# Optimization experiments

Hardware: AMD Instinct MI355X
Metric: run time of the kernel (lower is better)

The kernel has to match this reference:

```python
import jax, jax.numpy as jnp
import numpy as np

N_HEAD = 16

def setup_inputs() -> dict:
    key = jax.random.key(0)
    ks = jax.random.split(key, 6)
    C = 1024
    B, T, Tp = 8, 1024, 64
    s = 0.02
    return {
        "x": jax.random.normal(ks[0], (B, T, C), jnp.float32),
        "prefix_embd": jax.random.normal(ks[1], (B, Tp, C), jnp.float32),
        "w_attn": jax.random.normal(ks[2], (C, 3 * C), jnp.float32) * s,
        "b_attn": jnp.zeros((3 * C,), jnp.float32),
        "w_prefix": jax.random.normal(ks[3], (C, 3 * C), jnp.float32) * s,
        "b_prefix": jnp.zeros((3 * C,), jnp.float32),
        "w_proj": jax.random.normal(ks[4], (C, C), jnp.float32) * s,
        "b_proj": jnp.zeros((C,), jnp.float32),
    }

def _heads(t, H):
    B, T, C = t.shape
    return t.reshape(B, T, H, C // H).transpose(0, 2, 1, 3)  # (B,H,T,d)

def reference(x, prefix_embd, w_attn, b_attn, w_prefix, b_prefix, w_proj, b_proj):
    B, T, C = x.shape
    H = N_HEAD
    d = C // H
    Tp = prefix_embd.shape[1]
    scale = 1.0 / jnp.sqrt(jnp.asarray(d, x.dtype))

    qkv = x @ w_attn + b_attn
    q, k, v = (_heads(t, H) for t in jnp.split(qkv, 3, axis=2))  # (B,H,T,d)

    pqkv = prefix_embd @ w_prefix + b_prefix
    _, k_p, v_p = (_heads(t, H) for t in jnp.split(pqkv, 3, axis=2))  # (B,H,Tp,d)

    causal = jnp.tril(jnp.ones((T, T), bool))  # bias buffer slice
    neg_inf = jnp.asarray(float("-inf"), x.dtype)

    att = jnp.einsum("bhqd,bhkd->bhqk", q, k) * scale
    att = jnp.where(causal[None, None], att, neg_inf)
    att = jax.nn.softmax(att, axis=-1)

    att_p = jnp.einsum("bhqd,bhkd->bhqk", q, k_p) * scale
    att_p = jnp.where(causal[:, :Tp][None, None], att_p, neg_inf)
    att_p = jax.nn.softmax(att_p, axis=-1)

    y = jnp.einsum("bhqk,bhkd->bhqd", att_p, v_p) + jnp.einsum("bhqk,bhkd->bhqd", att, v)
    y = y.transpose(0, 2, 1, 3).reshape(B, T, C)
    return y @ w_proj + b_proj
```

## Files before the change

kernel.cpp:

```cpp
#include <hip/hip_runtime.h>
#include <hip/hip_bf16.h>
#include <cstdint>
#include <cstddef>

typedef __bf16 bf16_t;
typedef bf16_t bf16x8 __attribute__((ext_vector_type(8)));
typedef bf16_t bf16x4 __attribute__((ext_vector_type(4)));
typedef float f32x4 __attribute__((ext_vector_type(4)));

#define NB 8
#define NT 1024
#define NC 1024
#define NH 16
#define ND 64
#define NTP 64

__global__ __launch_bounds__(256) void k_cast2(const float* __restrict__ a, bf16_t* __restrict__ da,
                                               int n4a,
                                               const float* __restrict__ b2, bf16_t* __restrict__ db,
                                               int n4b) {
    int i = blockIdx.x * 256 + threadIdx.x;
    if (i < n4a) {
        float4 f = ((const float4*)a)[i];
        bf16x4 o;
        o[0] = (bf16_t)f.x; o[1] = (bf16_t)f.y; o[2] = (bf16_t)f.z; o[3] = (bf16_t)f.w;
        ((bf16x4*)da)[i] = o;
    } else {
        int j = i - n4a;
        if (j < n4b) {
            float4 f = ((const float4*)b2)[j];
            bf16x4 o;
            o[0] = (bf16_t)f.x; o[1] = (bf16_t)f.y; o[2] = (bf16_t)f.z; o[3] = (bf16_t)f.w;
            ((bf16x4*)db)[j] = o;
        }
    }
}

__global__ __launch_bounds__(256) void k_transpose3(const float* __restrict__ s0, bf16_t* __restrict__ d0,
                                                    const float* __restrict__ s1, bf16_t* __restrict__ d1,
                                                    const float* __restrict__ s2, bf16_t* __restrict__ d2) {
    __shared__ float tile[32][33];
    const int z = blockIdx.z;
    const float* src = (z == 0) ? s0 : (z == 1) ? s1 : s2;
    bf16_t* dst = (z == 0) ? d0 : (z == 1) ? d1 : d2;
    const int N = (z == 2) ? NC : 3 * NC;
    const int K = NC;
    if (z == 2 && blockIdx.x >= 32) return;
    int nt = blockIdx.x, kt = blockIdx.y;
    int tx = threadIdx.x & 31;
    int ty = threadIdx.x >> 5;
#pragma unroll
    for (int i = 0; i < 4; i++) {
        int r = ty + i * 8;
        tile[r][tx] = src[(size_t)(kt * 32 + r) * N + nt * 32 + tx];
    }
    __syncthreads();
#pragma unroll
    for (int i = 0; i < 4; i++) {
        int r = ty + i * 8;
        dst[(size_t)(nt * 32 + r) * K + kt * 32 + tx] = (bf16_t)tile[tx][r];
    }
}

template <int OMODE, int TSH>
__global__ __launch_bounds__(256) void k_gemm_f(const bf16_t* __restrict__ A,
                                                const bf16_t* __restrict__ BT,
                                                const float* __restrict__ bias,
                                                void* __restrict__ Cout,
                                                int M, int N, int K) {
    __shared__ bf16_t As[128 * 72];
    __shared__ bf16_t Bs[128 * 72];
    const int tid = threadIdx.x;
    const int lane = tid & 63;
    const int wave = tid >> 6;
    const int quad = lane >> 4;
    const int l15 = lane & 15;
    const int wm = (wave >> 1) * 64;
    const int wn = (wave & 1) * 64;
    const size_t rowA0 = (size_t)blockIdx.y * 128;
    const size_t colB0 = (size_t)blockIdx.x * 128;

    const f32x4 fz = {0.f, 0.f, 0.f, 0.f};
    f32x4 acc[4][4];
#pragma unroll
    for (int i = 0; i < 4; i++)
#pragma unroll
        for (int j = 0; j < 4; j++) acc[i][j] = fz;

    for (int k0 = 0; k0 < K; k0 += 64) {
        __syncthreads();
#pragma unroll
        for (int i = 0; i < 4; i++) {
            int c = tid + i * 256;
            int r = c >> 3;
            int kc = (c & 7) * 8;
            uint4 av = *(const uint4*)(A + (rowA0 + r) * (size_t)K + k0 + kc);
            *(uint4*)(&As[r * 72 + kc]) = av;
            uint4 bv = *(const uint4*)(BT + (colB0 + r) * (size_t)K + k0 + kc);
            *(uint4*)(&Bs[r * 72 + kc]) = bv;
        }
        __syncthreads();
#pragma unroll
        for (int kk = 0; kk < 2; kk++) {
            bf16x8 af[4], bfr[4];
#pragma unroll
            for (int i = 0; i < 4; i++)
                af[i] = *(const bf16x8*)(&As[(wm + i * 16 + l15) * 72 + kk * 32 + quad * 8]);
#pragma unroll
            for (int j = 0; j < 4; j++)
                bfr[j] = *(const bf16x8*)(&Bs[(wn + j * 16 + l15) * 72 + kk * 32 + quad * 8]);
#pragma unroll
            for (int i = 0; i < 4; i++)
#pragma unroll
                for (int j = 0; j < 4; j++)
                    acc[i][j] = __builtin_amdgcn_mfma_f32_16x16x32_bf16(af[i], bfr[j], acc[i][j], 0, 0, 0);
        }
    }
    const bool vpath = (OMODE == 2) && (colB0 >= (size_t)(2 * NC));
#pragma unroll
    for (int i = 0; i < 4; i++) {
        size_t row = rowA0 + wm + i * 16 + quad * 4;
#pragma unroll
        for (int j = 0; j < 4; j++) {
            int col = (int)colB0 + wn + j * 16 + l15;
            float bv = bias[col];
            if (vpath) {
                int hh = (col - 2 * NC) >> 6;
                int dd = col & 63;
                int bb = (int)(row >> TSH);
                int tt = (int)row & ((1 << TSH) - 1);
                int tileBase = (bb * NH + hh) * (1 << (TSH - 6)) + (tt >> 6);
                size_t chunkrow = (size_t)tileBase * 4 + (dd >> 4);
                size_t addr = chunkrow * (size_t)N + 2 * NC + (dd & 15) * 64 + (tt & 63);
                bf16x4 vv;
#pragma unroll
                for (int r = 0; r < 4; r++) vv[r] = (bf16_t)(acc[i][j][r] + bv);
                *(bf16x4*)((bf16_t*)Cout + addr) = vv;
            } else {
#pragma unroll
                for (int r = 0; r < 4; r++) {
                    float v = acc[i][j][r] + bv;
                    if (OMODE == 1)
                        ((float*)Cout)[(row + r) * (size_t)N + col] = v;
                    else
                        ((bf16_t*)Cout)[(row + r) * (size_t)N + col] = (bf16_t)v;
                }
            }
        }
    }
}


#define LOADREGS(KB, VCB)                                                            \
    rk0 = *(const uint4*)((KB) + (size_t)(tid >> 3) * 3072 + (tid & 7) * 8);         \
    rv0 = *(const uint4*)((VCB) + (size_t)(tid >> 7) * 3072 + (tid & 127) * 8);

#define STAGE(KS, VS)                                                \
    *(uint4*)(&(KS)[(tid >> 3) * 72 + (tid & 7) * 8]) = rk0;         \
    *(uint4*)(&(VS)[(tid >> 3) * 72 + (tid & 7) * 8]) = rv0;

#define QK(KS, Sj, j)                                                                  \
    Sj = __builtin_amdgcn_mfma_f32_16x16x32_bf16(                                      \
        aq0, *(const bf16x8*)(&(KS)[((j) * 16 + l15) * 72 + quad * 8]), Sj, 0, 0, 0);  \
    Sj = __builtin_amdgcn_mfma_f32_16x16x32_bf16(                                      \
        aq1, *(const bf16x8*)(&(KS)[((j) * 16 + l15) * 72 + 32 + quad * 8]), Sj, 0, 0, 0);

#define EXPJ(Sj, j, BL, LACC)                                           \
    {                                                                   \
        const int n_ = (j) * 16 + l15;                                  \
        _Pragma("unroll") for (int r_ = 0; r_ < 4; r_++) {              \
            float p_ = __expf(Sj[r_] * scale);                          \
            if (n_ > (BL) + r_) p_ = 0.f;                               \
            Sj[r_] = p_;                                                \
            LACC[r_] += p_;                                             \
        }                                                               \
    }

#define PSTORE(Sj, j)                                                   \
    _Pragma("unroll") for (int r_ = 0; r_ < 4; r_++)                    \
        P[(quad * 4 + r_) * 72 + (j) * 16 + l15] = (bf16_t)Sj[r_];

#define PV(VS, Oj, j)                                                                  \
    Oj = __builtin_amdgcn_mfma_f32_16x16x32_bf16(                                      \
        ap0, *(const bf16x8*)(&(VS)[((j) * 16 + l15) * 72 + quad * 8]), Oj, 0, 0, 0);  \
    Oj = __builtin_amdgcn_mfma_f32_16x16x32_bf16(                                      \
        ap1, *(const bf16x8*)(&(VS)[((j) * 16 + l15) * 72 + 32 + quad * 8]), Oj, 0, 0, 0);

#define PROC(KS, VS, BL, LACC, O0, O1, O2, O3)                          \
    {                                                                   \
        f32x4 S0 = fz, S1 = fz, S2 = fz, S3 = fz;                       \
        __builtin_amdgcn_s_setprio(1);                                  \
        QK(KS, S0, 0) QK(KS, S1, 1) QK(KS, S2, 2) QK(KS, S3, 3)         \
        __builtin_amdgcn_s_setprio(0);                                  \
        EXPJ(S0, 0, BL, LACC) EXPJ(S1, 1, BL, LACC)                     \
        EXPJ(S2, 2, BL, LACC) EXPJ(S3, 3, BL, LACC)                     \
        PSTORE(S0, 0) PSTORE(S1, 1) PSTORE(S2, 2) PSTORE(S3, 3)         \
        __builtin_amdgcn_s_waitcnt(0xc07f);             \
        __builtin_amdgcn_wave_barrier();                                \
        bf16x8 ap0 = *(const bf16x8*)(&P[l15 * 72 + quad * 8]);         \
        bf16x8 ap1 = *(const bf16x8*)(&P[l15 * 72 + 32 + quad * 8]);    \
        __builtin_amdgcn_s_setprio(1);                                  \
        PV(VS, O0, 0) PV(VS, O1, 1) PV(VS, O2, 2) PV(VS, O3, 3)         \
        __builtin_amdgcn_s_setprio(0);                                  \
    }

#define STORE_O(Oj, Pj, j)                                                            \
    _Pragma("unroll") for (int r_ = 0; r_ < 4; r_++) {                                \
        float v_ = Oj[r_] * lmv[r_] + Pj[r_] * lpv[r_];                               \
        y[(qrow0 + quad * 4 + r_) * NC + h * 64 + (j) * 16 + l15] = (bf16_t)v_;       \
    }

__global__ __launch_bounds__(512, 2) void k_attn11(const bf16_t* __restrict__ qkv,
                                                   const bf16_t* __restrict__ pqkv,
                                                   bf16_t* __restrict__ y) {
    const int qt = (NT / 128 - 1) - blockIdx.x;
    const int h = blockIdx.y;
    const int b = blockIdx.z;
    const int TMAX = 2 * qt + 1;

    __shared__ bf16_t Ks0[64 * 72], Ks1[64 * 72];
    __shared__ bf16_t Vs0[64 * 72], Vs1[64 * 72];
    __shared__ bf16_t Ps[8][16 * 72];

    const int tid = threadIdx.x;
    const int lane = tid & 63;
    const int wave = tid >> 6;
    const int quad = lane >> 4;
    const int l15 = lane & 15;
    const float scale = 0.125f;

    const size_t qrow0 = (size_t)b * NT + (size_t)qt * 128 + wave * 16;
    const int qoff = qt * 128 + wave * 16 + quad * 4;
    bf16_t* P = Ps[wave];

    const bf16_t* Kmain = qkv + (size_t)(b * NT) * 3072 + NC + h * 64;
    const bf16_t* Vmain = qkv + (size_t)(b * NH + h) * 16 * 4 * 3072 + 2 * NC;
    const bf16_t* Vpre  = pqkv + (size_t)(b * NH + h) * 4 * 3072 + 2 * NC;

    bf16x8 aq0 = *(const bf16x8*)(qkv + (qrow0 + l15) * 3072 + h * 64 + quad * 8);
    bf16x8 aq1 = *(const bf16x8*)(qkv + (qrow0 + l15) * 3072 + h * 64 + 32 + quad * 8);

    const f32x4 fz = {0.f, 0.f, 0.f, 0.f};
    f32x4 Om0 = fz, Om1 = fz, Om2 = fz, Om3 = fz;
    f32x4 Op0 = fz, Op1 = fz, Op2 = fz, Op3 = fz;
    f32x4 Lm = fz, Lp = fz;
    uint4 rk0, rv0;

    LOADREGS(pqkv + (size_t)(b * NTP) * 3072 + NC + h * 64, Vpre)
    STAGE(Ks0, Vs0)
    LOADREGS(Kmain, Vmain)
    __syncthreads();
    PROC(Ks0, Vs0, qoff, Lp, Op0, Op1, Op2, Op3)
    STAGE(Ks1, Vs1)
    LOADREGS(Kmain + (size_t)64 * 3072, Vmain + 4 * 3072)

    for (int t = 0; t <= TMAX; t++) {
        __syncthreads();
        bf16_t* KSc = (t & 1) ? Ks0 : Ks1;
        bf16_t* VSc = (t & 1) ? Vs0 : Vs1;
        if (t < TMAX) {
            bf16_t* KSn = (t & 1) ? Ks1 : Ks0;
            bf16_t* VSn = (t & 1) ? Vs1 : Vs0;
            STAGE(KSn, VSn)
        }
        if (t + 1 < TMAX) {
            LOADREGS(Kmain + ((size_t)(t + 2) * 64) * 3072, Vmain + (size_t)(t + 2) * 4 * 3072)
        }
        PROC(KSc, VSc, qoff - t * 64, Lm, Om0, Om1, Om2, Om3)
    }

    f32x4 lmv, lpv;
#pragma unroll
    for (int r = 0; r < 4; r++) {
        float vm = Lm[r], vpr = Lp[r];
#pragma unroll
        for (int off = 1; off < 16; off <<= 1) {
            vm += __shfl_xor(vm, off, 64);
            vpr += __shfl_xor(vpr, off, 64);
        }
        lmv[r] = 1.0f / vm;
        lpv[r] = 1.0f / vpr;
    }

    STORE_O(Om0, Op0, 0) STORE_O(Om1, Op1, 1) STORE_O(Om2, Op2, 2) STORE_O(Om3, Op3, 3)
}

extern "C" void kernel_launch(void* const* d_in, const int* in_sizes, int n_in,
                              void* d_out, int out_size, void* d_ws, size_t ws_size,
                              hipStream_t stream) {
    (void)in_sizes; (void)n_in; (void)out_size; (void)ws_size;
    const float* x        = (const float*)d_in[0];
    const float* prefix   = (const float*)d_in[1];
    const float* w_attn   = (const float*)d_in[2];
    const float* b_attn   = (const float*)d_in[3];
    const float* w_prefix = (const float*)d_in[4];
    const float* b_prefix = (const float*)d_in[5];
    const float* w_proj   = (const float*)d_in[6];
    const float* b_proj   = (const float*)d_in[7];
    float* out = (float*)d_out;

    char* p = (char*)d_ws;
    auto carve = [&](size_t bytes) {
        char* q = p;
        p += (bytes + 255) & ~(size_t)255;
        return q;
    };
    bf16_t* xb   = (bf16_t*)carve((size_t)NB * NT * NC * 2);
    bf16_t* pb   = (bf16_t*)carve((size_t)NB * NTP * NC * 2);
    bf16_t* wTa  = (bf16_t*)carve((size_t)3 * NC * NC * 2);
    bf16_t* wTp  = (bf16_t*)carve((size_t)3 * NC * NC * 2);
    bf16_t* wTpr = (bf16_t*)carve((size_t)NC * NC * 2);
    bf16_t* qkv  = (bf16_t*)carve((size_t)NB * NT * 3 * NC * 2);
    bf16_t* pqkv = (bf16_t*)carve((size_t)NB * NTP * 3 * NC * 2);
    bf16_t* yb   = (bf16_t*)carve((size_t)NB * NT * NC * 2);

    const int n4a = NB * NT * NC / 4, n4b = NB * NTP * NC / 4;
    k_cast2<<<(n4a + n4b + 255) / 256, 256, 0, stream>>>(x, xb, n4a, prefix, pb, n4b);
    k_transpose3<<<dim3(3 * NC / 32, NC / 32, 3), 256, 0, stream>>>(w_attn, wTa, w_prefix, wTp,
                                                                    w_proj, wTpr);
    k_gemm_f<2, 10><<<dim3(3 * NC / 128, NB * NT / 128), 256, 0, stream>>>(
        xb, wTa, b_attn, qkv, NB * NT, 3 * NC, NC);
    k_gemm_f<2, 6><<<dim3(3 * NC / 128, NB * NTP / 128), 256, 0, stream>>>(
        pb, wTp, b_prefix, pqkv, NB * NTP, 3 * NC, NC);
    k_attn11<<<dim3(NT / 128, NH, NB), 512, 0, stream>>>(qkv, pqkv, yb);
    k_gemm_f<1, 6><<<dim3(NC / 128, NB * NT / 128), 256, 0, stream>>>(
        yb, wTpr, b_proj, out, NB * NT, NC, NC);
}
```

Before: 307.9 us.

## Merge QKV and prefix GEMMs into one launch and remap workgroups across XCDs

Combines the main QKV projection and the prefix projection into a single GEMM launch of 24x68 workgroups, which removes one kernel launch and the tail of the small prefix GEMM. Workgroup IDs in the GEMMs and the attention kernel are remapped with a stride-8 swizzle so that neighbouring tiles land on the same XCD and share its L2. The tile shape sizes are unchanged; the cost is some extra index arithmetic and runtime branching on which GEMM a block handles.

```diff
diff --git a/kernel.cpp b/kernel.cpp
--- a/kernel.cpp
+++ b/kernel.cpp
@@ -62,12 +62,30 @@
     }
 }
 
-template <int OMODE, int TSH>
-__global__ __launch_bounds__(256) void k_gemm_f(const bf16_t* __restrict__ A,
-                                                const bf16_t* __restrict__ BT,
-                                                const float* __restrict__ bias,
-                                                void* __restrict__ Cout,
-                                                int M, int N, int K) {
+
+__global__ __launch_bounds__(256) void k_gemm_qkv(const bf16_t* __restrict__ xb,
+                                                  const bf16_t* __restrict__ pb,
+                                                  const bf16_t* __restrict__ wTa,
+                                                  const bf16_t* __restrict__ wTp,
+                                                  const float* __restrict__ b_attn,
+                                                  const float* __restrict__ b_prefix,
+                                                  bf16_t* __restrict__ qkv,
+                                                  bf16_t* __restrict__ pqkv) {
+    const int nwg = 24 * 68;
+    const int flat = blockIdx.y * 24 + blockIdx.x;
+    const int wgid = (flat & 7) * (nwg >> 3) + (flat >> 3);
+    const int bx = wgid % 24;
+    const int byw = wgid / 24;
+    const bool pre = (byw >= 64);
+    const bf16_t* A = pre ? pb : xb;
+    const bf16_t* BT = pre ? wTp : wTa;
+    const float* bias = pre ? b_prefix : b_attn;
+    bf16_t* Cout = pre ? pqkv : qkv;
+    const int tsh = pre ? 6 : 10;
+    const size_t rowA0 = (size_t)(pre ? (byw - 64) : byw) * 128;
+    const size_t colB0 = (size_t)bx * 128;
+    const int K = NC, N = 3 * NC;
+
     __shared__ bf16_t As[128 * 72];
     __shared__ bf16_t Bs[128 * 72];
     const int tid = threadIdx.x;
@@ -77,8 +95,6 @@
     const int l15 = lane & 15;
     const int wm = (wave >> 1) * 64;
     const int wn = (wave & 1) * 64;
-    const size_t rowA0 = (size_t)blockIdx.y * 128;
-    const size_t colB0 = (size_t)blockIdx.x * 128;
 
     const f32x4 fz = {0.f, 0.f, 0.f, 0.f};
     f32x4 acc[4][4];
@@ -116,7 +132,7 @@
                     acc[i][j] = __builtin_amdgcn_mfma_f32_16x16x32_bf16(af[i], bfr[j], acc[i][j], 0, 0, 0);
         }
     }
-    const bool vpath = (OMODE == 2) && (colB0 >= (size_t)(2 * NC));
+    const bool vpath = (colB0 >= (size_t)(2 * NC));
 #pragma unroll
     for (int i = 0; i < 4; i++) {
         size_t row = rowA0 + wm + i * 16 + quad * 4;
@@ -127,29 +143,98 @@
             if (vpath) {
                 int hh = (col - 2 * NC) >> 6;
                 int dd = col & 63;
-                int bb = (int)(row >> TSH);
-                int tt = (int)row & ((1 << TSH) - 1);
-                int tileBase = (bb * NH + hh) * (1 << (TSH - 6)) + (tt >> 6);
+                int bb = (int)(row >> tsh);
+                int tt = (int)row & ((1 << tsh) - 1);
+                int tileBase = (bb * NH + hh) * (1 << (tsh - 6)) + (tt >> 6);
                 size_t chunkrow = (size_t)tileBase * 4 + (dd >> 4);
                 size_t addr = chunkrow * (size_t)N + 2 * NC + (dd & 15) * 64 + (tt & 63);
                 bf16x4 vv;
 #pragma unroll
                 for (int r = 0; r < 4; r++) vv[r] = (bf16_t)(acc[i][j][r] + bv);
-                *(bf16x4*)((bf16_t*)Cout + addr) = vv;
+                *(bf16x4*)(Cout + addr) = vv;
             } else {
 #pragma unroll
                 for (int r = 0; r < 4; r++) {
                     float v = acc[i][j][r] + bv;
-                    if (OMODE == 1)
-                        ((float*)Cout)[(row + r) * (size_t)N + col] = v;
-                    else
-                        ((bf16_t*)Cout)[(row + r) * (size_t)N + col] = (bf16_t)v;
+                    Cout[(row + r) * (size_t)N + col] = (bf16_t)v;
                 }
             }
         }
     }
 }
 
+__global__ __launch_bounds__(256) void k_gemm_proj(const bf16_t* __restrict__ A,
+                                                   const bf16_t* __restrict__ BT,
+                                                   const float* __restrict__ bias,
+                                                   float* __restrict__ Cout,
+                                                   int M, int N, int K) {
+    const int nwg = gridDim.x * gridDim.y;
+    const int flat = blockIdx.y * gridDim.x + blockIdx.x;
+    const int wgid = (flat & 7) * (nwg >> 3) + (flat >> 3);
+    const int bx = wgid % gridDim.x;
+    const int byw = wgid / gridDim.x;
+    const size_t rowA0 = (size_t)byw * 128;
+    const size_t colB0 = (size_t)bx * 128;
+
+    __shared__ bf16_t As[128 * 72];
+    __shared__ bf16_t Bs[128 * 72];
+    const int tid = threadIdx.x;
+    const int lane = tid & 63;
+    const int wave = tid >> 6;
+    const int quad = lane >> 4;
+    const int l15 = lane & 15;
+    const int wm = (wave >> 1) * 64;
+    const int wn = (wave & 1) * 64;
+
+    const f32x4 fz = {0.f, 0.f, 0.f, 0.f};
+    f32x4 acc[4][4];
+#pragma unroll
+    for (int i = 0; i < 4; i++)
+#pragma unroll
+        for (int j = 0; j < 4; j++) acc[i][j] = fz;
+
+    for (int k0 = 0; k0 < K; k0 += 64) {
+        __syncthreads();
+#pragma unroll
+        for (int i = 0; i < 4; i++) {
+            int c = tid + i * 256;
+            int r = c >> 3;
+            int kc = (c & 7) * 8;
+            uint4 av = *(const uint4*)(A + (rowA0 + r) * (size_t)K + k0 + kc);
+            *(uint4*)(&As[r * 72 + kc]) = av;
+            uint4 bv = *(const uint4*)(BT + (colB0 + r) * (size_t)K + k0 + kc);
+            *(uint4*)(&Bs[r * 72 + kc]) = bv;
+        }
+        __syncthreads();
+#pragma unroll
+        for (int kk = 0; kk < 2; kk++) {
+            bf16x8 af[4], bfr[4];
+#pragma unroll
+            for (int i = 0; i < 4; i++)
+                af[i] = *(const bf16x8*)(&As[(wm + i * 16 + l15) * 72 + kk * 32 + quad * 8]);
+#pragma unroll
+            for (int j = 0; j < 4; j++)
+                bfr[j] = *(const bf16x8*)(&Bs[(wn + j * 16 + l15) * 72 + kk * 32 + quad * 8]);
+#pragma unroll
+            for (int i = 0; i < 4; i++)
+#pragma unroll
+                for (int j = 0; j < 4; j++)
+                    acc[i][j] = __builtin_amdgcn_mfma_f32_16x16x32_bf16(af[i], bfr[j], acc[i][j], 0, 0, 0);
+        }
+    }
+#pragma unroll
+    for (int i = 0; i < 4; i++) {
+        size_t row = rowA0 + wm + i * 16 + quad * 4;
+#pragma unroll
+        for (int j = 0; j < 4; j++) {
+            int col = (int)colB0 + wn + j * 16 + l15;
+            float bv = bias[col];
+#pragma unroll
+            for (int r = 0; r < 4; r++)
+                Cout[(row + r) * (size_t)N + col] = acc[i][j][r] + bv;
+        }
+    }
+}
 
 #define LOADREGS(KB, VCB)                                                            \
     rk0 = *(const uint4*)((KB) + (size_t)(tid >> 3) * 3072 + (tid & 7) * 8);         \
@@ -213,9 +298,11 @@
 __global__ __launch_bounds__(512, 2) void k_attn11(const bf16_t* __restrict__ qkv,
                                                    const bf16_t* __restrict__ pqkv,
                                                    bf16_t* __restrict__ y) {
-    const int qt = (NT / 128 - 1) - blockIdx.x;
-    const int h = blockIdx.y;
-    const int b = blockIdx.z;
+    const int flat = (int)blockIdx.x + 8 * ((int)blockIdx.y + 16 * (int)blockIdx.z);
+    const int wgid = (flat & 7) * 128 + (flat >> 3);
+    const int qt = (NT / 128 - 1) - (wgid & 7);
+    const int h = (wgid >> 3) & 15;
+    const int b = wgid >> 7;
     const int TMAX = 2 * qt + 1;
 
     __shared__ bf16_t Ks0[64 * 72], Ks1[64 * 72];
@@ -318,11 +405,8 @@
     k_cast2<<<(n4a + n4b + 255) / 256, 256, 0, stream>>>(x, xb, n4a, prefix, pb, n4b);
     k_transpose3<<<dim3(3 * NC / 32, NC / 32, 3), 256, 0, stream>>>(w_attn, wTa, w_prefix, wTp,
                                                                     w_proj, wTpr);
-    k_gemm_f<2, 10><<<dim3(3 * NC / 128, NB * NT / 128), 256, 0, stream>>>(
-        xb, wTa, b_attn, qkv, NB * NT, 3 * NC, NC);
-    k_gemm_f<2, 6><<<dim3(3 * NC / 128, NB * NTP / 128), 256, 0, stream>>>(
-        pb, wTp, b_prefix, pqkv, NB * NTP, 3 * NC, NC);
+    k_gemm_qkv<<<dim3(24, 68), 256, 0, stream>>>(xb, pb, wTa, wTp, b_attn, b_prefix, qkv, pqkv);
     k_attn11<<<dim3(NT / 128, NH, NB), 512, 0, stream>>>(qkv, pqkv, yb);
-    k_gemm_f<1, 6><<<dim3(NC / 128, NB * NT / 128), 256, 0, stream>>>(
+    k_gemm_proj<<<dim3(NC / 128, NB * NT / 128), 256, 0, stream>>>(
         yb, wTpr, b_proj, out, NB * NT, NC, NC);
 }
```

Result: faster. 298.2 us (-3.1%).
